# Performance work log

Hardware: AMD Instinct MI355X
Metric: run time of the kernel (lower is better)

The kernel has to match this reference:

```python
import jax, jax.numpy as jnp
import numpy as np

SEGMENT_LENGTHS = [1024, 2048, 4096]
DILATION_RATES = [1, 2, 4]


def setup_inputs() -> dict:
    key = jax.random.key(0)
    kq, kk, kv = jax.random.split(key, 3)
    shape = (2, 4096, 12, 64)  # (batch, seq_len, num_heads, head_dim)
    return {
        "q": jax.random.normal(kq, shape, dtype=jnp.float32),
        "k": jax.random.normal(kk, shape, dtype=jnp.float32),
        "v": jax.random.normal(kv, shape, dtype=jnp.float32),
        "is_causal": 0,
    }


def _group_attention(qg, kg, vg, L, dil_rate, is_causal, scale):
    # qg/kg/vg: [b, n, hg, d]; block-local attention with block size L.
    # NOTE: the original _get_dilated_indices degenerates to the identity
    # segment slice (i=0 row fills all L indices before truncation), so the
    # dilated gather equals the contiguous segment for any dilation_rate.
    b, n, hg, d = qg.shape
    ns = n // L
    q_ = qg.reshape(b, ns, L, hg, d)
    k_ = kg.reshape(b, ns, L, hg, d)
    v_ = vg.reshape(b, ns, L, hg, d)
    scores = jnp.einsum("bsqhd,bskhd->bshqk", q_, k_) * scale  # [b,ns,hg,L,L]
    if is_causal and dil_rate == 1:
        # causal mask is applied only to segment 0 in the original
        causal = jnp.tril(jnp.ones((L, L), dtype=bool))  # [L,L]
        seg0 = (jnp.arange(ns) == 0)[None, :, None, None, None]  # [1,ns,1,1,1]
        neg = jnp.asarray(jnp.finfo(scores.dtype).min, scores.dtype)
        scores = jnp.where(seg0 & ~causal[None, None, None], neg, scores)
    attn = jax.nn.softmax(scores, axis=-1)
    out = jnp.einsum("bshqk,bskhd->bsqhd", attn, v_)
    return out.reshape(b, n, hg, d)


def reference(q, k, v, is_causal):
    b, n, h, d = q.shape
    num_groups = len(SEGMENT_LENGTHS)
    hg = h // num_groups
    scale = 1.0 / (float(d) ** 0.5)
    outs = []
    for gi, (L, r) in enumerate(zip(SEGMENT_LENGTHS, DILATION_RATES)):
        hs = gi * hg
        he = (gi + 1) * hg if gi < num_groups - 1 else h
        outs.append(
            _group_attention(
                q[:, :, hs:he], k[:, :, hs:he], v[:, :, hs:he],
                L, r, bool(is_causal), scale,
            )
        )
    return jnp.concatenate(outs, axis=2)  # [b, n, h, d]
```

## Files before the change

### kernel.cpp

```cpp
#include <hip/hip_runtime.h>
#include <hip/hip_bf16.h>

typedef __bf16 bf16;
typedef _Float16 f16;
typedef __attribute__((ext_vector_type(2))) __bf16 bf16x2;
typedef __attribute__((ext_vector_type(4))) __bf16 bf16x4;
typedef __attribute__((ext_vector_type(8))) __bf16 bf16x8;
typedef __attribute__((ext_vector_type(4))) _Float16 f16x4;
typedef __attribute__((ext_vector_type(8))) _Float16 f16x8;
typedef __attribute__((ext_vector_type(4))) float f32x4;
typedef __attribute__((ext_vector_type(16))) float f32x16;
typedef __attribute__((ext_vector_type(4))) unsigned u32x4;

#define SW(row, col) ((col) ^ (((row) & 7) << 3))

#define GL16(g, l) __builtin_amdgcn_global_load_lds( \
    (const __attribute__((address_space(1))) void*)(g), \
    (__attribute__((address_space(3))) void*)(l), 16, 0, 0)

static __device__ __forceinline__ unsigned pkbf(float a, float b) {
    bf16x2 t = { (bf16)a, (bf16)b };
    return __builtin_bit_cast(unsigned, t);
}

__global__ __launch_bounds__(256) void prep_fused(
    const float* __restrict__ k, const float* __restrict__ v,
    bf16* __restrict__ Kb, bf16* __restrict__ Vt)
{
    __shared__ bf16 T[64][72];
    const int bid = (int)blockIdx.x;
    const int tid = threadIdx.x;
    if (bid < 6144) {
        const size_t i = ((size_t)bid * 256 + tid) * 4;
        float4 f = *(const float4*)(k + i);
        bf16x4 o = { (bf16)f.x, (bf16)f.y, (bf16)f.z, (bf16)f.w };
        *(bf16x4*)(Kb + i) = o;
        return;
    }
    const int vb  = bid - 6144;
    const int n64 = vb & 63;
    const int bh  = vb >> 6;
    const int b   = bh / 12, h = bh - b * 12;
    {
        const int i  = tid >> 2;
        const int dc = (tid & 3) << 4;
        const float* vp = v + (size_t)(b * 4096 + (n64 << 6) + i) * 768 + h * 64 + dc;
        float tv[16];
#pragma unroll
        for (int j2 = 0; j2 < 4; ++j2) *(float4*)&tv[j2 * 4] = ((const float4*)vp)[j2];
#pragma unroll
        for (int j = 0; j < 16; ++j) T[dc + j][i] = (bf16)tv[j];
    }
    __syncthreads();
    {
        const int d  = tid >> 2;
        const int nc = (tid & 3) << 4;
        bf16* op = Vt + (size_t)(bh * 64 + d) * 4096 + (n64 << 6) + nc;
        *(bf16x8*)op       = *(const bf16x8*)&T[d][nc];
        *(bf16x8*)(op + 8) = *(const bf16x8*)&T[d][nc + 8];
    }
}

__global__ __launch_bounds__(256, 3) void dila_attn32(
    const float* __restrict__ q, const bf16* __restrict__ Kb,
    const bf16* __restrict__ Vt, const int* __restrict__ causal_p,
    float* __restrict__ out, f16* __restrict__ Opart, float* __restrict__ lpart)
{
    __shared__ bf16 Ksh[2][64][64];
    __shared__ bf16 Vsh[2][64][64];

    const int tid  = threadIdx.x;
    const int lane = tid & 63;
    const int w    = tid >> 6;
    const int l31  = lane & 31;
    const int h5   = lane >> 5;

    const int bid = (int)blockIdx.x;
    int h, b, qc, so, nt, sp = 0, gslot = -1;
    bool cflag = false;
    if (bid < 512) {
        h = 8 + (bid >> 7);
        const int r = bid & 127; sp = r >> 6;
        const int r2 = r & 63; b = r2 >> 5; qc = r2 & 31;
        so = sp << 11; nt = 32;
        gslot = (h - 8) * 64 + b * 32 + qc;
    } else if (bid < 768) {
        const int i = bid - 512;
        h = 4 + (i >> 6);
        const int r = i & 63; b = r >> 5; qc = r & 31;
        so = (qc >> 4) << 11; nt = 32;
    } else {
        const int i = bid - 768;
        h = i >> 7;
        const int r = i & 127; sp = r >> 6;
        const int r2 = r & 63; b = r2 >> 5; qc = r2 & 31;
        so = ((qc >> 3) << 10) + (sp << 9); nt = 8; cflag = true;
        gslot = 256 + h * 64 + b * 32 + qc;
    }
    const int q0 = qc << 7;
    const bool causal = cflag && ((qc >> 3) == 0) && (*causal_p != 0);
    const int qg = q0 + (w << 5) + l31;

    const float QS = 0.125f * 1.44269504088896340736f;
    const float* qrp = q + (size_t)(b * 4096 + qg) * 768 + h * 64 + (h5 << 3);
    bf16x8 qf[4];
#pragma unroll
    for (int c = 0; c < 4; ++c) {
        float tq[8];
        *(float4*)&tq[0] = *(const float4*)(qrp + 16 * c);
        *(float4*)&tq[4] = *(const float4*)(qrp + 16 * c + 4);
        bf16x8 t;
#pragma unroll
        for (int j = 0; j < 8; ++j) t[j] = (bf16)(tq[j] * QS);
        qf[c] = t;
    }

    f32x16 o0 = (f32x16)(0.f), o1 = (f32x16)(0.f);
    float lreg = 0.f;

    const int rK = lane >> 3;
    const int gK = (lane & 7) ^ rK;
    const bf16* kp = Kb + (size_t)(b * 4096 + so + (w << 4) + rK) * 768 + h * 64 + gK * 8;
    const bf16* vp = Vt + (size_t)((b * 12 + h) * 64 + (w << 4) + rK) * 4096 + so + gK * 8;

    {
        bf16* kd = &Ksh[0][w << 4][0];
        bf16* vd = &Vsh[0][w << 4][0];
        GL16(kp, kd); GL16(kp + 8 * 768, kd + 512);
        GL16(vp, vd); GL16(vp + 8 * 4096, vd + 512);
        kp += 64 * 768; vp += 64;
    }

    for (int t = 0; t < nt; ++t) {
        const int buf = t & 1;
        __builtin_amdgcn_s_barrier();
        if (t + 1 < nt) {
            bf16* kd = &Ksh[buf ^ 1][w << 4][0];
            bf16* vd = &Vsh[buf ^ 1][w << 4][0];
            GL16(kp, kd); GL16(kp + 8 * 768, kd + 512);
            GL16(vp, vd); GL16(vp + 8 * 4096, vd + 512);
            kp += 64 * 768; vp += 64;
            asm volatile("s_waitcnt vmcnt(4)" ::: "memory");
        } else {
            asm volatile("s_waitcnt vmcnt(0)" ::: "memory");
        }
        __builtin_amdgcn_s_barrier();

        const bf16 (*Kc)[64] = Ksh[buf];
        const bf16 (*Vc)[64] = Vsh[buf];

        f32x16 s0 = (f32x16)(-12.0f), s1 = (f32x16)(-12.0f);
        __builtin_amdgcn_s_setprio(1);
#pragma unroll
        for (int c = 0; c < 4; ++c) {
            const int col = (c << 4) + (h5 << 3);
            bf16x8 kf0 = *(const bf16x8*)&Kc[l31][SW(l31, col)];
            bf16x8 kf1 = *(const bf16x8*)&Kc[32 + l31][SW(32 + l31, col)];
            s0 = __builtin_amdgcn_mfma_f32_32x32x16_bf16(kf0, qf[c], s0, 0, 0, 0);
            s1 = __builtin_amdgcn_mfma_f32_32x32x16_bf16(kf1, qf[c], s1, 0, 0, 0);
        }
        __builtin_amdgcn_s_setprio(0);

        if (causal) {
#pragma unroll
            for (int reg = 0; reg < 16; ++reg) {
                const int kr = (reg & 3) + ((reg >> 2) << 3) + (h5 << 2);
                if (so + (t << 6) + kr > qg)      s0[reg] = -1e30f;
                if (so + (t << 6) + 32 + kr > qg) s1[reg] = -1e30f;
            }
        }

        float p0[16], p1[16], rs = 0.f;
#pragma unroll
        for (int reg = 0; reg < 16; ++reg) {
            p0[reg] = __builtin_amdgcn_exp2f(s0[reg]);
            p1[reg] = __builtin_amdgcn_exp2f(s1[reg]);
            rs += p0[reg] + p1[reg];
        }
        lreg += rs;

        unsigned pk[8][2];
#pragma unroll
        for (int rr = 0; rr < 4; ++rr) {
            pk[rr][0]     = pkbf(p0[4 * rr + 0], p0[4 * rr + 1]);
            pk[rr][1]     = pkbf(p0[4 * rr + 2], p0[4 * rr + 3]);
            pk[4 + rr][0] = pkbf(p1[4 * rr + 0], p1[4 * rr + 1]);
            pk[4 + rr][1] = pkbf(p1[4 * rr + 2], p1[4 * rr + 3]);
        }
        bf16x8 pf[4];
#pragma unroll
        for (int c = 0; c < 4; ++c) {
            unsigned X0 = pk[2 * c][0],     X1 = pk[2 * c][1];
            unsigned Y0 = pk[2 * c + 1][0], Y1 = pk[2 * c + 1][1];
            asm("v_permlane32_swap_b32 %0, %1" : "+v"(X0), "+v"(Y0));
            asm("v_permlane32_swap_b32 %0, %1" : "+v"(X1), "+v"(Y1));
            u32x4 fu = { X0, X1, Y0, Y1 };
            pf[c] = __builtin_bit_cast(bf16x8, fu);
        }

        __builtin_amdgcn_s_setprio(1);
#pragma unroll
        for (int c = 0; c < 4; ++c) {
            const int col = (c << 4) + (h5 << 3);
            bf16x8 vf0 = *(const bf16x8*)&Vc[l31][SW(l31, col)];
            bf16x8 vf1 = *(const bf16x8*)&Vc[32 + l31][SW(32 + l31, col)];
            o0 = __builtin_amdgcn_mfma_f32_32x32x16_bf16(vf0, pf[c], o0, 0, 0, 0);
            o1 = __builtin_amdgcn_mfma_f32_32x32x16_bf16(vf1, pf[c], o1, 0, 0, 0);
        }
        __builtin_amdgcn_s_setprio(0);
    }

    const float lt = lreg + __shfl_xor(lreg, 32);
    const int qloc = (w << 5) + l31;
    if (gslot < 0) {
        const float inv = 1.0f / lt;
        float* op = out + (size_t)(b * 4096 + q0 + qloc) * 768 + h * 64;
#pragma unroll
        for (int rr = 0; rr < 4; ++rr) {
            const int d0 = (rr << 3) + (h5 << 2);
            float4 a = { o0[4 * rr] * inv, o0[4 * rr + 1] * inv, o0[4 * rr + 2] * inv, o0[4 * rr + 3] * inv };
            float4 c = { o1[4 * rr] * inv, o1[4 * rr + 1] * inv, o1[4 * rr + 2] * inv, o1[4 * rr + 3] * inv };
            *(float4*)&op[d0]      = a;
            *(float4*)&op[32 + d0] = c;
        }
    } else if (sp == 0) {
        float* op = out + (size_t)(b * 4096 + q0 + qloc) * 768 + h * 64;
#pragma unroll
        for (int rr = 0; rr < 4; ++rr) {
            const int d0 = (rr << 3) + (h5 << 2);
            float4 a = { o0[4 * rr], o0[4 * rr + 1], o0[4 * rr + 2], o0[4 * rr + 3] };
            float4 c = { o1[4 * rr], o1[4 * rr + 1], o1[4 * rr + 2], o1[4 * rr + 3] };
            *(float4*)&op[d0]      = a;
            *(float4*)&op[32 + d0] = c;
        }
        if (h5 == 0) lpart[gslot * 256 + qloc] = lt;
    } else {
        f16* os = Opart + (size_t)gslot * 8192 + qloc * 64;
#pragma unroll
        for (int rr = 0; rr < 4; ++rr) {
            const int d0 = (rr << 3) + (h5 << 2);
            f16x4 a = { (f16)o0[4 * rr], (f16)o0[4 * rr + 1], (f16)o0[4 * rr + 2], (f16)o0[4 * rr + 3] };
            f16x4 c = { (f16)o1[4 * rr], (f16)o1[4 * rr + 1], (f16)o1[4 * rr + 2], (f16)o1[4 * rr + 3] };
            *(f16x4*)&os[d0]      = a;
            *(f16x4*)&os[32 + d0] = c;
        }
        if (h5 == 0) lpart[gslot * 256 + 128 + qloc] = lt;
    }
}

__global__ __launch_bounds__(256) void reduce_splits(
    const f16* __restrict__ Opart, const float* __restrict__ lpart,
    float* __restrict__ out)
{
    const int g = (int)blockIdx.x;
    int h, b, qc;
    if (g < 256) { h = 8 + (g >> 6); b = (g >> 5) & 1; qc = g & 31; }
    else { const int g2 = g - 256; h = g2 >> 6; b = (g2 >> 5) & 1; qc = g2 & 31; }
    const int t = threadIdx.x;
    const int row = t >> 1;
    const int dh = (t & 1) << 5;
    const f16* s1 = Opart + (size_t)g * 8192 + row * 64 + dh;
    const float inv = 1.0f / (lpart[g * 256 + row] + lpart[g * 256 + 128 + row]);
    float* op = out + (size_t)(b * 4096 + (qc << 7) + row) * 768 + h * 64 + dh;
#pragma unroll
    for (int j = 0; j < 32; j += 8) {
        float4 a0 = *(const float4*)(op + j);
        float4 a1 = *(const float4*)(op + j + 4);
        f16x8 c = *(const f16x8*)(s1 + j);
        float4 r0 = { (a0.x + (float)c[0]) * inv, (a0.y + (float)c[1]) * inv,
                      (a0.z + (float)c[2]) * inv, (a0.w + (float)c[3]) * inv };
        float4 r1 = { (a1.x + (float)c[4]) * inv, (a1.y + (float)c[5]) * inv,
                      (a1.z + (float)c[6]) * inv, (a1.w + (float)c[7]) * inv };
        *(float4*)(op + j)     = r0;
        *(float4*)(op + j + 4) = r1;
    }
}

__global__ __launch_bounds__(256) void dila_attn_legacy(
    const float* __restrict__ q, const float* __restrict__ k,
    const float* __restrict__ v, const int* __restrict__ causal_p,
    float* __restrict__ out)
{
    __shared__ bf16 Ksh[64][64];
    __shared__ bf16 Vsh[64][64];
    __shared__ bf16 Psh[4][16][72];

    const int tid  = threadIdx.x;
    const int lane = tid & 63;
    const int wid  = tid >> 6;
    const int lm   = lane & 15;
    const int lg   = lane >> 4;

    const int h   = 11 - (int)(blockIdx.x >> 7);
    const int rem = (int)(blockIdx.x & 127);
    const int b   = rem >> 6;
    const int qb  = rem & 63;

    const int grp = h >> 2;
    const int L   = 1024 << grp;
    const int q0  = qb << 6;
    const int seg = q0 / L;
    const int kv0 = seg * L;
    const int nt  = L >> 6;
    const bool causal = (grp == 0) && (seg == 0) && (*causal_p != 0);

    const float* qb_p = q   + (size_t)b * 4096 * 768 + h * 64;
    const float* kb_p = k   + (size_t)b * 4096 * 768 + h * 64;
    const float* vb_p = v   + (size_t)b * 4096 * 768 + h * 64;
    float*       ob_p = out + (size_t)b * 4096 * 768 + h * 64;

    const float QSCALE = 0.125f * 1.44269504088896340736f;
    const int qrow = q0 + (wid << 4) + lm;
    const float* qp = qb_p + (size_t)qrow * 768 + (lg << 3);
    bf16x8 qf[2];
#pragma unroll
    for (int kc = 0; kc < 2; ++kc) {
        float tq[8];
        *(float4*)&tq[0] = ((const float4*)(qp + kc * 32))[0];
        *(float4*)&tq[4] = ((const float4*)(qp + kc * 32))[1];
        bf16x8 tt;
#pragma unroll
        for (int j = 0; j < 8; ++j) tt[j] = (bf16)(tq[j] * QSCALE);
        qf[kc] = tt;
    }

    f32x4 o[4];
#pragma unroll
    for (int i = 0; i < 4; ++i) o[i] = (f32x4){0.f, 0.f, 0.f, 0.f};
    float mrun = -1e30f, lrun = 0.f;

    const int sr = tid >> 2;
    const int sc = (tid & 3) << 4;
    const int vbr = tid >> 4;
    const int vbc = tid & 15;

    const float* kp0 = kb_p + (size_t)(kv0 + sr) * 768 + sc;
    const float* vp0 = vb_p + (size_t)(kv0 + (vbr << 2)) * 768 + (vbc << 2);

    for (int t = 0; t < nt; ++t) {
        {
            const float* kp = kp0 + (size_t)t * (64 * 768);
            float tk[16];
#pragma unroll
            for (int i = 0; i < 4; ++i) *(float4*)&tk[4 * i] = ((const float4*)kp)[i];
            bf16x8 c0, c1;
#pragma unroll
            for (int j = 0; j < 8; ++j) { c0[j] = (bf16)tk[j]; c1[j] = (bf16)tk[8 + j]; }
            *(bf16x8*)&Ksh[sr][SW(sr, sc)]     = c0;
            *(bf16x8*)&Ksh[sr][SW(sr, sc + 8)] = c1;
        }
        {
            const float* vp = vp0 + (size_t)t * (64 * 768);
            float4 tv[4];
#pragma unroll
            for (int i = 0; i < 4; ++i) tv[i] = *(const float4*)(vp + (size_t)i * 768);
#pragma unroll
            for (int jc = 0; jc < 4; ++jc) {
                const int d = (vbc << 2) + jc;
                bf16x4 wv = { (bf16)((&tv[0].x)[jc]), (bf16)((&tv[1].x)[jc]),
                              (bf16)((&tv[2].x)[jc]), (bf16)((&tv[3].x)[jc]) };
                *(bf16x4*)&Vsh[d][SW(d, vbr << 2)] = wv;
            }
        }
        __syncthreads();

        f32x4 s[4];
#pragma unroll
        for (int cb = 0; cb < 4; ++cb) {
            f32x4 acc = (f32x4){0.f, 0.f, 0.f, 0.f};
            const int krow = (cb << 4) + lm;
#pragma unroll
            for (int kc = 0; kc < 2; ++kc) {
                bf16x8 kf = *(const bf16x8*)&Ksh[krow][SW(krow, (lg << 3) + (kc << 5))];
                acc = __builtin_amdgcn_mfma_f32_16x16x32_bf16(kf, qf[kc], acc, 0, 0, 0);
            }
            s[cb] = acc;
        }

        if (causal) {
            const int qg = q0 + (wid << 4) + lm;
#pragma unroll
            for (int cb = 0; cb < 4; ++cb) {
                const int kbase = kv0 + (t << 6) + (cb << 4) + (lg << 2);
#pragma unroll
                for (int r = 0; r < 4; ++r)
                    if (kbase + r > qg) s[cb][r] = -1e30f;
            }
        }

        {
            float mx = fmaxf(fmaxf(fmaxf(s[0][0], s[0][1]), fmaxf(s[0][2], s[0][3])),
                             fmaxf(fmaxf(s[1][0], s[1][1]), fmaxf(s[1][2], s[1][3])));
            float mx2 = fmaxf(fmaxf(fmaxf(s[2][0], s[2][1]), fmaxf(s[2][2], s[2][3])),
                              fmaxf(fmaxf(s[3][0], s[3][1]), fmaxf(s[3][2], s[3][3])));
            mx = fmaxf(mx, mx2);
            mx = fmaxf(mx, __shfl_xor(mx, 16));
            mx = fmaxf(mx, __shfl_xor(mx, 32));
            const float mn = fmaxf(mrun, mx);
            const float cr = __builtin_amdgcn_exp2f(mrun - mn);
            mrun = mn;
            float rs = 0.f;
#pragma unroll
            for (int cb = 0; cb < 4; ++cb) {
                f32x4 pp;
#pragma unroll
                for (int r = 0; r < 4; ++r) {
                    pp[r] = __builtin_amdgcn_exp2f(s[cb][r] - mn);
                    rs += pp[r];
                }
                bf16x4 wv = { (bf16)pp[0], (bf16)pp[1], (bf16)pp[2], (bf16)pp[3] };
                *(bf16x4*)&Psh[wid][lm][(cb << 4) + (lg << 2)] = wv;
            }
            rs += __shfl_xor(rs, 16);
            rs += __shfl_xor(rs, 32);
            lrun = lrun * cr + rs;
#pragma unroll
            for (int db = 0; db < 4; ++db)
#pragma unroll
                for (int r = 0; r < 4; ++r) o[db][r] *= cr;
        }

        {
            bf16x8 pfr[2];
#pragma unroll
            for (int kc = 0; kc < 2; ++kc)
                pfr[kc] = *(const bf16x8*)&Psh[wid][lm][(lg << 3) + (kc << 5)];
#pragma unroll
            for (int db = 0; db < 4; ++db) {
                const int vr = (db << 4) + lm;
#pragma unroll
                for (int kc = 0; kc < 2; ++kc) {
                    bf16x8 vf = *(const bf16x8*)&Vsh[vr][SW(vr, (lg << 3) + (kc << 5))];
                    o[db] = __builtin_amdgcn_mfma_f32_16x16x32_bf16(vf, pfr[kc], o[db], 0, 0, 0);
                }
            }
        }
        __syncthreads();
    }

    {
        const float inv = 1.0f / lrun;
        const int orow = q0 + (wid << 4) + lm;
        float* op = ob_p + (size_t)orow * 768 + (lg << 2);
#pragma unroll
        for (int db = 0; db < 4; ++db) {
            float4 wv = { o[db][0] * inv, o[db][1] * inv, o[db][2] * inv, o[db][3] * inv };
            *(float4*)(op + (db << 4)) = wv;
        }
    }
}

extern "C" void kernel_launch(void* const* d_in, const int* in_sizes, int n_in,
                              void* d_out, int out_size, void* d_ws, size_t ws_size,
                              hipStream_t stream) {
    const float* q = (const float*)d_in[0];
    const float* k = (const float*)d_in[1];
    const float* v = (const float*)d_in[2];
    const int* causal_p = (const int*)d_in[3];
    float* out = (float*)d_out;

    const size_t elems = (size_t)2 * 4096 * 12 * 64;
    const size_t kb_b  = elems * sizeof(bf16);
    const size_t vt_b  = elems * sizeof(bf16);
    const size_t op_b  = (size_t)512 * 8192 * sizeof(f16);
    const size_t lp_b  = (size_t)512 * 256 * sizeof(float);
    const size_t need  = kb_b + vt_b + op_b + lp_b;

    if (ws_size >= need) {
        bf16* Kb    = (bf16*)d_ws;
        bf16* Vt    = Kb + elems;
        f16*  Opart = (f16*)(Vt + elems);
        float* lpart = (float*)((char*)Opart + op_b);
        prep_fused<<<dim3(7680), dim3(256), 0, stream>>>(k, v, Kb, Vt);
        dila_attn32<<<dim3(1280), dim3(256), 0, stream>>>(q, Kb, Vt, causal_p, out, Opart, lpart);
        reduce_splits<<<dim3(512), dim3(256), 0, stream>>>(Opart, lpart, out);
    } else {
        dila_attn_legacy<<<dim3(1536), dim3(256), 0, stream>>>(q, k, v, causal_p, out);
    }
}
```

Measured before the change: 103.2 us.

## Add 32-key-tile attention kernel with per-group split-KV and multi-split reduce

Adds a new attention kernel that processes 32-key tiles instead of 64. It splits the KV range of the 2048- and 4096-length head groups into 1024-key chunks, giving 1792 blocks that each do the same amount of work, while the 1024 group writes directly. A new reduce kernel merges the 4-way and 2-way splits. The aim is better load balance and more blocks across the CUs. In exchange it needs a larger workspace and adds more partial-output traffic, with softmax computed without a max subtraction (fixed offset).

```diff
diff --git a/kernel.cpp b/kernel.cpp
--- a/kernel.cpp
+++ b/kernel.cpp
@@ -58,6 +58,228 @@
         bf16* op = Vt + (size_t)(bh * 64 + d) * 4096 + (n64 << 6) + nc;
         *(bf16x8*)op       = *(const bf16x8*)&T[d][nc];
         *(bf16x8*)(op + 8) = *(const bf16x8*)&T[d][nc + 8];
+    }
+}
+
+__global__ __launch_bounds__(256, 3) void attn_kv32(
+    const float* __restrict__ q, const bf16* __restrict__ Kb,
+    const bf16* __restrict__ Vt, const int* __restrict__ causal_p,
+    float* __restrict__ out, f16* __restrict__ Opart, float* __restrict__ lpart)
+{
+    __shared__ bf16 Ksh[2][32][64];
+    __shared__ bf16 Vsh[2][64][32];
+
+    const int tid  = threadIdx.x;
+    const int lane = tid & 63;
+    const int w    = tid >> 6;
+    const int l31  = lane & 31;
+    const int h5   = lane >> 5;
+
+    const int bid = (int)blockIdx.x;
+    int h, b, qc, so, sp = 0, lbase = 0, oslot = 0;
+    bool direct = false, cflag = false;
+    if (bid < 1024) {
+        h = 8 + (bid >> 8);
+        const int r = bid & 255; sp = r >> 6;
+        const int r2 = r & 63; b = r2 >> 5; qc = r2 & 31;
+        so = sp << 10;
+        const int gi = (h - 8) * 64 + b * 32 + qc;
+        lbase = gi * 4; oslot = gi * 3 + (sp - 1);
+    } else if (bid < 1536) {
+        const int i = bid - 1024;
+        h = 4 + (i >> 7);
+        const int r = i & 127; sp = r >> 6;
+        const int r2 = r & 63; b = r2 >> 5; qc = r2 & 31;
+        so = ((qc >> 4) << 11) + (sp << 10);
+        const int gi = (h - 4) * 64 + b * 32 + qc;
+        lbase = 1024 + gi * 2; oslot = 768 + gi;
+    } else {
+        const int i = bid - 1536;
+        h = i >> 6;
+        const int r = i & 63; b = r >> 5; qc = r & 31;
+        so = (qc >> 3) << 10; direct = true; cflag = true;
+    }
+    const int q0 = qc << 7;
+    const bool causal = cflag && ((qc >> 3) == 0) && (*causal_p != 0);
+    const int qg = q0 + (w << 5) + l31;
+
+    const float QS = 0.125f * 1.44269504088896340736f;
+    const float* qrp = q + (size_t)(b * 4096 + qg) * 768 + h * 64 + (h5 << 3);
+    bf16x8 qf[4];
+#pragma unroll
+    for (int c = 0; c < 4; ++c) {
+        float tq[8];
+        *(float4*)&tq[0] = *(const float4*)(qrp + 16 * c);
+        *(float4*)&tq[4] = *(const float4*)(qrp + 16 * c + 4);
+        bf16x8 t;
+#pragma unroll
+        for (int j = 0; j < 8; ++j) t[j] = (bf16)(tq[j] * QS);
+        qf[c] = t;
+    }
+
+    f32x16 o0 = (f32x16)(0.f), o1 = (f32x16)(0.f);
+    float lreg = 0.f;
+
+    const int rk  = tid >> 3;
+    const int gk  = (tid & 7) ^ (rk & 7);
+    const int dv  = tid >> 2;
+    const int gv  = (tid & 3) ^ (dv & 3);
+    const bf16* kp = Kb + (size_t)(b * 4096 + so + rk) * 768 + h * 64 + gk * 8;
+    const bf16* vp = Vt + (size_t)((b * 12 + h) * 64 + dv) * 4096 + so + gv * 8;
+
+    {
+        GL16(kp, &Ksh[0][w << 3][0]);
+        GL16(vp, &Vsh[0][w << 4][0]);
+        kp += 32 * 768; vp += 32;
+    }
+
+    for (int t = 0; t < 32; ++t) {
+        const int buf = t & 1;
+        __builtin_amdgcn_s_barrier();
+        if (t < 31) {
+            GL16(kp, &Ksh[buf ^ 1][w << 3][0]);
+            GL16(vp, &Vsh[buf ^ 1][w << 4][0]);
+            kp += 32 * 768; vp += 32;
+            asm volatile("s_waitcnt vmcnt(2)" ::: "memory");
+        } else {
+            asm volatile("s_waitcnt vmcnt(0)" ::: "memory");
+        }
+        __builtin_amdgcn_s_barrier();
+
+        const bf16 (*Kc)[64] = Ksh[buf];
+        const bf16 (*Vc)[32] = Vsh[buf];
+
+        f32x16 s0 = (f32x16)(-12.0f);
+        __builtin_amdgcn_s_setprio(1);
+#pragma unroll
+        for (int c = 0; c < 4; ++c) {
+            const int col = (c << 4) + (h5 << 3);
+            bf16x8 kf = *(const bf16x8*)&Kc[l31][SW(l31, col)];
+            s0 = __builtin_amdgcn_mfma_f32_32x32x16_bf16(kf, qf[c], s0, 0, 0, 0);
+        }
+        __builtin_amdgcn_s_setprio(0);
+
+        if (causal) {
+#pragma unroll
+            for (int reg = 0; reg < 16; ++reg) {
+                const int kr = (reg & 3) + ((reg >> 2) << 3) + (h5 << 2);
+                if (so + (t << 5) + kr > qg) s0[reg] = -1e30f;
+            }
+        }
+
+        float rs0 = 0.f, rs1 = 0.f;
+#pragma unroll
+        for (int reg = 0; reg < 16; ++reg) {
+            s0[reg] = __builtin_amdgcn_exp2f(s0[reg]);
+            if (reg & 1) rs1 += s0[reg]; else rs0 += s0[reg];
+        }
+        lreg += rs0 + rs1;
+
+        unsigned pk[4][2];
+#pragma unroll
+        for (int g = 0; g < 4; ++g) {
+            pk[g][0] = pkbf(s0[4 * g + 0], s0[4 * g + 1]);
+            pk[g][1] = pkbf(s0[4 * g + 2], s0[4 * g + 3]);
+        }
+        bf16x8 pf[2];
+#pragma unroll
+        for (int c = 0; c < 2; ++c) {
+            unsigned X0 = pk[2 * c][0],     X1 = pk[2 * c][1];
+            unsigned Y0 = pk[2 * c + 1][0], Y1 = pk[2 * c + 1][1];
+            asm("v_permlane32_swap_b32 %0, %1" : "+v"(X0), "+v"(Y0));
+            asm("v_permlane32_swap_b32 %0, %1" : "+v"(X1), "+v"(Y1));
+            u32x4 fu = { X0, X1, Y0, Y1 };
+            pf[c] = __builtin_bit_cast(bf16x8, fu);
+        }
+
+        __builtin_amdgcn_s_setprio(1);
+#pragma unroll
+        for (int c = 0; c < 2; ++c) {
+            const int col = (c << 4) + (h5 << 3);
+            bf16x8 vf0 = *(const bf16x8*)&Vc[l31][col ^ ((l31 & 3) << 3)];
+            bf16x8 vf1 = *(const bf16x8*)&Vc[32 + l31][col ^ ((l31 & 3) << 3)];
+            o0 = __builtin_amdgcn_mfma_f32_32x32x16_bf16(vf0, pf[c], o0, 0, 0, 0);
+            o1 = __builtin_amdgcn_mfma_f32_32x32x16_bf16(vf1, pf[c], o1, 0, 0, 0);
+        }
+        __builtin_amdgcn_s_setprio(0);
+    }
+
+    const float lt = lreg + __shfl_xor(lreg, 32);
+    const int qloc = (w << 5) + l31;
+    if (direct) {
+        const float inv = 1.0f / lt;
+        float* op = out + (size_t)(b * 4096 + q0 + qloc) * 768 + h * 64;
+#pragma unroll
+        for (int rr = 0; rr < 4; ++rr) {
+            const int d0 = (rr << 3) + (h5 << 2);
+            float4 a = { o0[4 * rr] * inv, o0[4 * rr + 1] * inv, o0[4 * rr + 2] * inv, o0[4 * rr + 3] * inv };
+            float4 c = { o1[4 * rr] * inv, o1[4 * rr + 1] * inv, o1[4 * rr + 2] * inv, o1[4 * rr + 3] * inv };
+            *(float4*)&op[d0]      = a;
+            *(float4*)&op[32 + d0] = c;
+        }
+    } else {
+        if (h5 == 0) lpart[(size_t)(lbase + sp) * 128 + qloc] = lt;
+        if (sp == 0) {
+            float* op = out + (size_t)(b * 4096 + q0 + qloc) * 768 + h * 64;
+#pragma unroll
+            for (int rr = 0; rr < 4; ++rr) {
+                const int d0 = (rr << 3) + (h5 << 2);
+                float4 a = { o0[4 * rr], o0[4 * rr + 1], o0[4 * rr + 2], o0[4 * rr + 3] };
+                float4 c = { o1[4 * rr], o1[4 * rr + 1], o1[4 * rr + 2], o1[4 * rr + 3] };
+                *(float4*)&op[d0]      = a;
+                *(float4*)&op[32 + d0] = c;
+            }
+        } else {
+            f16* os = Opart + (size_t)oslot * 8192 + qloc * 64;
+#pragma unroll
+            for (int rr = 0; rr < 4; ++rr) {
+                const int d0 = (rr << 3) + (h5 << 2);
+                f16x4 a = { (f16)o0[4 * rr], (f16)o0[4 * rr + 1], (f16)o0[4 * rr + 2], (f16)o0[4 * rr + 3] };
+                f16x4 c = { (f16)o1[4 * rr], (f16)o1[4 * rr + 1], (f16)o1[4 * rr + 2], (f16)o1[4 * rr + 3] };
+                *(f16x4*)&os[d0]      = a;
+                *(f16x4*)&os[32 + d0] = c;
+            }
+        }
+    }
+}
+
+__global__ __launch_bounds__(256) void reduce_multi(
+    const f16* __restrict__ Opart, const float* __restrict__ lpart,
+    float* __restrict__ out)
+{
+    const int g = (int)blockIdx.x;
+    int h, b, qc, nsp, lbase, sbase, nslots;
+    if (g < 256) {
+        h = 8 + (g >> 6); b = (g >> 5) & 1; qc = g & 31;
+        nsp = 4; lbase = g * 4; sbase = g * 3; nslots = 3;
+    } else {
+        const int gi = g - 256;
+        h = 4 + (gi >> 6); b = (gi >> 5) & 1; qc = gi & 31;
+        nsp = 2; lbase = 1024 + gi * 2; sbase = 768 + gi; nslots = 1;
+    }
+    const int t = threadIdx.x;
+    const int row = t >> 1;
+    const int dh = (t & 1) << 5;
+    float l = 0.f;
+    for (int s = 0; s < nsp; ++s) l += lpart[(size_t)(lbase + s) * 128 + row];
+    const float inv = 1.0f / l;
+    float* op = out + (size_t)(b * 4096 + (qc << 7) + row) * 768 + h * 64 + dh;
+#pragma unroll
+    for (int j = 0; j < 32; j += 8) {
+        float acc[8];
+        float4 a0 = *(const float4*)(op + j);
+        float4 a1 = *(const float4*)(op + j + 4);
+        acc[0] = a0.x; acc[1] = a0.y; acc[2] = a0.z; acc[3] = a0.w;
+        acc[4] = a1.x; acc[5] = a1.y; acc[6] = a1.z; acc[7] = a1.w;
+        for (int s = 0; s < nslots; ++s) {
+            f16x8 c = *(const f16x8*)(Opart + (size_t)(sbase + s) * 8192 + row * 64 + dh + j);
+#pragma unroll
+            for (int e = 0; e < 8; ++e) acc[e] += (float)c[e];
+        }
+        float4 r0 = { acc[0] * inv, acc[1] * inv, acc[2] * inv, acc[3] * inv };
+        float4 r1 = { acc[4] * inv, acc[5] * inv, acc[6] * inv, acc[7] * inv };
+        *(float4*)(op + j)     = r0;
+        *(float4*)(op + j + 4) = r1;
     }
 }
 
@@ -462,15 +684,28 @@
     const size_t elems = (size_t)2 * 4096 * 12 * 64;
     const size_t kb_b  = elems * sizeof(bf16);
     const size_t vt_b  = elems * sizeof(bf16);
-    const size_t op_b  = (size_t)512 * 8192 * sizeof(f16);
-    const size_t lp_b  = (size_t)512 * 256 * sizeof(float);
-    const size_t need  = kb_b + vt_b + op_b + lp_b;
-
-    if (ws_size >= need) {
+
+    const size_t opP_b = (size_t)1024 * 8192 * sizeof(f16);
+    const size_t lpP_b = (size_t)1536 * 128 * sizeof(float);
+    const size_t needP = kb_b + vt_b + opP_b + lpP_b;
+
+    const size_t opF_b = (size_t)512 * 8192 * sizeof(f16);
+    const size_t lpF_b = (size_t)512 * 256 * sizeof(float);
+    const size_t needF = kb_b + vt_b + opF_b + lpF_b;
+
+    if (ws_size >= needP) {
         bf16* Kb    = (bf16*)d_ws;
         bf16* Vt    = Kb + elems;
         f16*  Opart = (f16*)(Vt + elems);
-        float* lpart = (float*)((char*)Opart + op_b);
+        float* lpart = (float*)((char*)Opart + opP_b);
+        prep_fused<<<dim3(7680), dim3(256), 0, stream>>>(k, v, Kb, Vt);
+        attn_kv32<<<dim3(1792), dim3(256), 0, stream>>>(q, Kb, Vt, causal_p, out, Opart, lpart);
+        reduce_multi<<<dim3(512), dim3(256), 0, stream>>>(Opart, lpart, out);
+    } else if (ws_size >= needF) {
+        bf16* Kb    = (bf16*)d_ws;
+        bf16* Vt    = Kb + elems;
+        f16*  Opart = (f16*)(Vt + elems);
+        float* lpart = (float*)((char*)Opart + opF_b);
         prep_fused<<<dim3(7680), dim3(256), 0, stream>>>(k, v, Kb, Vt);
         dila_attn32<<<dim3(1280), dim3(256), 0, stream>>>(q, Kb, Vt, causal_p, out, Opart, lpart);
         reduce_splits<<<dim3(512), dim3(256), 0, stream>>>(Opart, lpart, out);
```

Result: slower. 114.2 us (+10.7%).
